# Kernel tuning notes

Measured on AMD Instinct MI355X. Metric: run time of the kernel, lower is better.

## Reference

```python
import jax, jax.numpy as jnp
import numpy as np

C = 512; HEADS = 4; HD = C // HEADS
WS = (5, 9); EXP = (2, 4); FW = (5, 9)
SCALE = HD ** -0.5
B, T, NH, NW = 1, 5, 60, 108

def _valid_ind_rolled():
    wh, ww = WS; eh, ew = EXP
    tl = np.ones((wh, ww)); tl[:-eh, :-ew] = 0
    tr = np.ones((wh, ww)); tr[:-eh, ew:] = 0
    bl = np.ones((wh, ww)); bl[eh:, :-ew] = 0
    br = np.ones((wh, ww)); br[eh:, ew:] = 0
    return np.nonzero(np.stack([tl, tr, bl, br], 0).reshape(-1))[0]

VIR = jnp.asarray(_valid_ind_rolled())  # 120 valid rolled positions

def window_partition(x):
    b, t, h, w, c = x.shape
    x = x.reshape(b, t, h // WS[0], WS[0], w // WS[1], WS[1], c)
    return x.transpose(0, 2, 4, 1, 3, 5, 6).reshape(-1, t * WS[0] * WS[1], c)

def unfold(x, ker, pad):
    # torch.nn.Unfold(kernel=ker, stride=1, padding=pad): (n,c,h,w)->(n,c*kh*kw,L)
    n, c, h, w = x.shape
    xp = jnp.pad(x, ((0, 0), (0, 0), (pad[0], pad[0]), (pad[1], pad[1])))
    oh = h + 2 * pad[0] - ker[0] + 1
    ow = w + 2 * pad[1] - ker[1] + 1
    rows = jnp.arange(oh)[:, None] + jnp.arange(ker[0])[None, :]
    cols = jnp.arange(ow)[:, None] + jnp.arange(ker[1])[None, :]
    p = xp[:, :, rows[:, None, :, None], cols[None, :, None, :]]  # (n,c,oh,ow,kh,kw)
    return p.transpose(0, 1, 4, 5, 2, 3).reshape(n, c * ker[0] * ker[1], oh * ow)

def setup_inputs():
    key = jax.random.key(0)
    ks = jax.random.split(key, 4)
    return {
        "x0": jax.random.normal(ks[0], (B, T, NH, NW, C), jnp.float32),
        "x1": jax.random.normal(ks[1], (B, NH // WS[0], NW // WS[1], T, C), jnp.float32),
        "W_qkv": jax.random.normal(ks[2], (C, 3 * C), jnp.float32) * 0.02,
        "b_qkv": jnp.zeros((3 * C,), jnp.float32),
        "W_proj": jax.random.normal(ks[3], (C, C), jnp.float32) * 0.02,
        "b_proj": jnp.zeros((C,), jnp.float32),
    }

def reference(x0, x1, W_qkv, b_qkv, W_proj, b_proj):
    b, t, nh, nw, c = x0.shape
    wa = t * WS[0] * WS[1]  # tokens per window (225)
    qkv = (x0 @ W_qkv + b_qkv).reshape(b, t, nh, nw, 3, c)
    q, k, v = qkv[..., 0, :], qkv[..., 1, :], qkv[..., 2, :]

    def to_win(z):
        w = window_partition(z).reshape(-1, t, WS[0] * WS[1], HEADS, HD)
        return w.transpose(0, 3, 1, 2, 4).reshape(-1, HEADS, wa, HD)

    q_w, k_w, v_w = to_win(q), to_win(k), to_win(v)

    shifts = [(-EXP[0], -EXP[1]), (-EXP[0], EXP[1]), (EXP[0], -EXP[1]), (EXP[0], EXP[1])]
    def rolled(z):
        parts = [window_partition(jnp.roll(z, s, axis=(2, 3))).reshape(-1, t, WS[0] * WS[1], HEADS, HD) for s in shifts]
        r = jnp.concatenate(parts, axis=2).transpose(0, 3, 1, 2, 4)[:, :, :, VIR]
        return r.reshape(-1, HEADS, t * VIR.shape[0], HD)

    k_rolled = jnp.concatenate([k_w, rolled(k)], 2)
    v_rolled = jnp.concatenate([v_w, rolled(v)], 2)

    # focal level 1 pooling (focal_level=2 -> single unfold level, stride 1)
    xp = x1.transpose(0, 3, 1, 2, 4)  # (B,T,nWh,nWw,C)
    nwh, nww = xp.shape[2], xp.shape[3]
    ker = (2 * (FW[0] // 2) + 1, 2 * (FW[1] // 2) + 1)  # (5,9)
    pad = (ker[0] // 2, ker[1] // 2)
    L = nwh * nww; kk = ker[0] * ker[1]
    um = unfold(jnp.ones((t, 1, nwh, nww), x0.dtype), ker, pad)  # (T,kk,L)
    um = um.reshape(1, t, ker[0], ker[1], L).transpose(4, 1, 2, 3, 0).reshape(L, t * kk)
    pool_mask = jnp.where(um == 0, jnp.float32(-100.0), jnp.float32(0.0))  # (L, T*kk)

    qkv_p = (xp @ W_qkv + b_qkv).reshape(b, t, nwh, nww, 3, c).transpose(4, 0, 1, 5, 2, 3).reshape(3, b * t, c, nwh, nww)
    def pooled(z):
        u = unfold(z, ker, pad).reshape(b, t, c, ker[0], ker[1], L).transpose(0, 5, 1, 3, 4, 2)
        u = u.reshape(-1, t, kk, HEADS, HD).transpose(0, 3, 1, 2, 4)
        return u.reshape(-1, HEADS, t * kk, HD)

    k_all = jnp.concatenate([k_rolled, pooled(qkv_p[1])], 2)
    v_all = jnp.concatenate([v_rolled, pooled(qkv_p[2])], 2)

    attn = jnp.einsum('bhqd,bhkd->bhqk', q_w * SCALE, k_all)
    offset = k_rolled.shape[2]
    pm = jnp.tile(pool_mask[None], (b, 1, 1)).reshape(-1, t * kk)[:, None, None, :]
    attn = attn.at[:, :, :, offset:].add(pm)
    attn = jax.nn.softmax(attn, axis=-1)
    out = jnp.einsum('bhqk,bhkd->bqhd', attn, v_all).reshape(attn.shape[0], wa, c)
    return out @ W_proj + b_proj
```

## Files before the change

kernel.cpp:

```cpp
#include <hip/hip_runtime.h>

typedef _Float16 h16;
typedef __attribute__((ext_vector_type(8))) _Float16 half8;
typedef __attribute__((ext_vector_type(2))) _Float16 half2v;
typedef __attribute__((ext_vector_type(4))) float float4v;

typedef const __attribute__((address_space(1))) unsigned char gu8;
typedef __attribute__((address_space(3))) unsigned char su8;

#define NTOK  32400
#define NPTOK 720
#define CDIM  512
#define SCALE 0.08838834764831845f
#define ZROW  NTOK
#define PROW  (NTOK + 1)

__constant__ int VIR_TBL[120] = {
  5,6,7,8, 14,15,16,17, 23,24,25,26,
  27,28,29,30,31,32,33,34,35, 36,37,38,39,40,41,42,43,44,
  45,46,47,48, 54,55,56,57, 63,64,65,66,
  72,73,74,75,76,77,78,79,80, 81,82,83,84,85,86,87,88,89,
  90,91,92,93,94,95,96,97,98, 99,100,101,102,103,104,105,106,107,
  113,114,115,116, 122,123,124,125, 131,132,133,134,
  135,136,137,138,139,140,141,142,143, 144,145,146,147,148,149,150,151,152,
  153,154,155,156, 162,163,164,165, 171,172,173,174
};

__global__ __launch_bounds__(256) void build_tok(int* __restrict__ Tok,
                                                 int* __restrict__ WMask,
                                                 h16* __restrict__ Kz,
                                                 h16* __restrict__ Vz) {
  const int win = blockIdx.x;
  const int wy = win / 12, wx = win % 12;
  if (win == 0) {
    for (int k = threadIdx.x; k < 512; k += 256) {
      Kz[(size_t)ZROW * CDIM + k] = (h16)0.f;
      Vz[(size_t)ZROW * CDIM + k] = (h16)0.f;
    }
  }
  for (int kidx = threadIdx.x; kidx < 1056; kidx += 256) {
    int e;
    if (kidx < 225) {
      int t = kidx / 45, pos = kidx % 45;
      int y = wy * 5 + pos / 9, x = wx * 9 + pos % 9;
      e = (t * 60 + y) * 108 + x;
    } else if (kidx < 825) {
      int jj = kidx - 225;
      int t = jj / 120, m = jj % 120;
      int vir = VIR_TBL[m];
      int p = vir / 45, pos = vir % 45;
      int r = pos / 9, c = pos % 9;
      int sy = (p < 2) ? -2 : 2;
      int sx = (p & 1) ? 4 : -4;
      int y = (wy * 5 + r - sy + 60) % 60;
      int x = (wx * 9 + c - sx + 108) % 108;
      e = (t * 60 + y) * 108 + x;
    } else if (kidx < 1050) {
      int jp = kidx - 825;
      int t = jp / 45, pos = jp % 45;
      int py = wy + pos / 9 - 2;
      int px = wx + pos % 9 - 4;
      e = (py >= 0 && py < 12 && px >= 0 && px < 12)
            ? (PROW + t * 144 + py * 12 + px) : ZROW;
    } else {
      e = ZROW;
    }
    Tok[win * 1056 + kidx] = e;
  }
  if (threadIdx.x < 33) {
    int m = 0;
#pragma unroll 1
    for (int r = 0; r < 32; r++) {
      int kidx = threadIdx.x * 32 + r;
      bool v;
      if (kidx < 825) v = true;
      else if (kidx < 1050) {
        int jp = kidx - 825, pos = jp % 45;
        int py = wy + pos / 9 - 2, px = wx + pos % 9 - 4;
        v = (py >= 0 && py < 12 && px >= 0 && px < 12);
      } else v = false;
      m |= (v ? 1 : 0) << r;
    }
    WMask[win * 33 + threadIdx.x] = m;
  }
}

__global__ __launch_bounds__(256) void transpose_cvt(const float* __restrict__ src,
                                                     h16* __restrict__ dst,
                                                     int R, int C) {
  __shared__ float T[32][33];
  const int t = threadIdx.x;
  const int ct = blockIdx.x * 32;
  const int rt = blockIdx.y * 32;
  const int c = t & 31, r0 = (t >> 5) * 4;
#pragma unroll
  for (int i = 0; i < 4; i++)
    T[r0 + i][c] = src[(size_t)(rt + r0 + i) * C + ct + c];
  __syncthreads();
#pragma unroll
  for (int i = 0; i < 4; i++)
    dst[(size_t)(ct + r0 + i) * R + rt + c] = (h16)T[c][r0 + i];
}

__global__ __launch_bounds__(256) void cvt_x0(const float* __restrict__ src,
                                              h16* __restrict__ dst) {
  const int total = NTOK * CDIM / 8;
  for (int i = blockIdx.x * 256 + threadIdx.x; i < total; i += gridDim.x * 256) {
    const float4* s = (const float4*)(src + (size_t)i * 8);
    float4 f0 = s[0], f1 = s[1];
    half8 h;
    h[0] = (h16)f0.x; h[1] = (h16)f0.y; h[2] = (h16)f0.z; h[3] = (h16)f0.w;
    h[4] = (h16)f1.x; h[5] = (h16)f1.y; h[6] = (h16)f1.z; h[7] = (h16)f1.w;
    *(half8*)(dst + (size_t)i * 8) = h;
  }
}

struct __align__(16) Stage2 { h16 Ah[2][128][32]; h16 Bh[2][128][32]; };
union __align__(16) GemmLDSQ { Stage2 s; h16 Cs[128][136]; };

__global__ __launch_bounds__(256) void gemm_qkv_mfma(
    const h16* __restrict__ A, const h16* __restrict__ Bt,
    const float* __restrict__ bias,
    h16* __restrict__ Q, h16* __restrict__ K, h16* __restrict__ V)
{
  __shared__ GemmLDSQ u;
  const int tid = threadIdx.x;
  const int lane = tid & 63, wv = tid >> 6;
  const int col = lane & 15, quad = lane >> 4;
  const int bn = blockIdx.x, bm = blockIdx.y;
  const int mo = (wv & 1) * 64, no = (wv >> 1) * 64;

  float4v acc[4][4];
#pragma unroll
  for (int i = 0; i < 4; i++)
#pragma unroll
    for (int j = 0; j < 4; j++) acc[i][j] = (float4v){0.f, 0.f, 0.f, 0.f};

  const int lrow = lane >> 2;
  const int lcol = (((lane & 3) ^ ((lane >> 3) & 3)) * 8);
  const int arow = bm * 128 + wv * 32 + lrow;
  const int ar = arow < NTOK ? arow : (NTOK - 1);
  const int ar2 = (arow + 16) < NTOK ? (arow + 16) : (NTOK - 1);
  const h16* Ag  = A + (size_t)ar * 512 + lcol;
  const h16* Ag2 = A + (size_t)ar2 * 512 + lcol;
  const h16* Bg  = Bt + (size_t)(bn * 128 + wv * 32 + lrow) * 512 + lcol;

#define STAGE_G(buf, k0) do {                                              \
    su8* Al = (su8*)&u.s.Ah[buf][wv * 32][0];                              \
    su8* Bl = (su8*)&u.s.Bh[buf][wv * 32][0];                              \
    __builtin_amdgcn_global_load_lds((gu8*)(Ag + (k0)),            Al,        16, 0, 0); \
    __builtin_amdgcn_global_load_lds((gu8*)(Ag2 + (k0)),           Al + 1024, 16, 0, 0); \
    __builtin_amdgcn_global_load_lds((gu8*)(Bg + (k0)),            Bl,        16, 0, 0); \
    __builtin_amdgcn_global_load_lds((gu8*)(Bg + (k0) + 16 * 512), Bl + 1024, 16, 0, 0); \
  } while (0)

  const int fsw = (quad ^ ((col >> 1) & 3)) * 8;
  STAGE_G(0, 0);
  __syncthreads();
  for (int kt = 0; kt < 16; kt++) {
    const int cur = kt & 1;
    if (kt + 1 < 16) STAGE_G(cur ^ 1, (kt + 1) * 32);

    half8 afr[4], bfr[4];
#pragma unroll
    for (int i = 0; i < 4; i++)
      afr[i] = *(const half8*)&u.s.Ah[cur][mo + i * 16 + col][fsw];
#pragma unroll
    for (int j = 0; j < 4; j++)
      bfr[j] = *(const half8*)&u.s.Bh[cur][no + j * 16 + col][fsw];
#pragma unroll
    for (int i = 0; i < 4; i++)
#pragma unroll
      for (int j = 0; j < 4; j++)
        acc[i][j] = __builtin_amdgcn_mfma_f32_16x16x32_f16(afr[i], bfr[j], acc[i][j], 0, 0, 0);
    __syncthreads();
  }

  float bv[4];
#pragma unroll
  for (int j = 0; j < 4; j++) bv[j] = bias[bn * 128 + no + j * 16 + col];
#pragma unroll
  for (int i = 0; i < 4; i++)
#pragma unroll
    for (int j = 0; j < 4; j++)
#pragma unroll
      for (int r = 0; r < 4; r++)
        u.Cs[mo + i * 16 + quad * 4 + r][no + j * 16 + col] = (h16)(acc[i][j][r] + bv[j]);
  __syncthreads();

  const int row_l = tid >> 1, halfseg = (tid & 1) * 64;
  const int row_g = bm * 128 + row_l;
  const int jsel = bn >> 2;
  const int ch0 = (bn & 3) * 128 + halfseg;
  h16* dst = (jsel == 0) ? Q : (jsel == 1) ? K : V;
  if (row_g < NTOK) {
#pragma unroll
    for (int c = 0; c < 64; c += 8)
      *(half8*)&dst[(size_t)row_g * 512 + ch0 + c] = *(const half8*)&u.Cs[row_l][halfseg + c];
  }
}

__global__ __launch_bounds__(256) void gemm_proj_mfma(
    const h16* __restrict__ A, const h16* __restrict__ Bt,
    const float* __restrict__ bias, float* __restrict__ out)
{
  __shared__ Stage2 s;
  const int tid = threadIdx.x;
  const int lane = tid & 63, wv = tid >> 6;
  const int col = lane & 15, quad = lane >> 4;
  const int bn = blockIdx.x, bm = blockIdx.y;
  const int mo = (wv & 1) * 64, no = (wv >> 1) * 64;

  float4v acc[4][4];
#pragma unroll
  for (int i = 0; i < 4; i++)
#pragma unroll
    for (int j = 0; j < 4; j++) acc[i][j] = (float4v){0.f, 0.f, 0.f, 0.f};

  const int lrow = lane >> 2;
  const int lcol = (((lane & 3) ^ ((lane >> 3) & 3)) * 8);
  const int arow = bm * 128 + wv * 32 + lrow;
  const int ar = arow < NTOK ? arow : (NTOK - 1);
  const int ar2 = (arow + 16) < NTOK ? (arow + 16) : (NTOK - 1);
  const h16* Ag  = A + (size_t)ar * 512 + lcol;
  const h16* Ag2 = A + (size_t)ar2 * 512 + lcol;
  const h16* Bg  = Bt + (size_t)(bn * 128 + wv * 32 + lrow) * 512 + lcol;

#define STAGE_P(buf, k0) do {                                              \
    su8* Al = (su8*)&s.Ah[buf][wv * 32][0];                                \
    su8* Bl = (su8*)&s.Bh[buf][wv * 32][0];                                \
    __builtin_amdgcn_global_load_lds((gu8*)(Ag + (k0)),            Al,        16, 0, 0); \
    __builtin_amdgcn_global_load_lds((gu8*)(Ag2 + (k0)),           Al + 1024, 16, 0, 0); \
    __builtin_amdgcn_global_load_lds((gu8*)(Bg + (k0)),            Bl,        16, 0, 0); \
    __builtin_amdgcn_global_load_lds((gu8*)(Bg + (k0) + 16 * 512), Bl + 1024, 16, 0, 0); \
  } while (0)

  const int fsw = (quad ^ ((col >> 1) & 3)) * 8;
  STAGE_P(0, 0);
  __syncthreads();
  for (int kt = 0; kt < 16; kt++) {
    const int cur = kt & 1;
    if (kt + 1 < 16) STAGE_P(cur ^ 1, (kt + 1) * 32);

    half8 afr[4], bfr[4];
#pragma unroll
    for (int i = 0; i < 4; i++)
      afr[i] = *(const half8*)&s.Ah[cur][mo + i * 16 + col][fsw];
#pragma unroll
    for (int j = 0; j < 4; j++)
      bfr[j] = *(const half8*)&s.Bh[cur][no + j * 16 + col][fsw];
#pragma unroll
    for (int i = 0; i < 4; i++)
#pragma unroll
      for (int j = 0; j < 4; j++)
        acc[i][j] = __builtin_amdgcn_mfma_f32_16x16x32_f16(afr[i], bfr[j], acc[i][j], 0, 0, 0);
    __syncthreads();
  }

  float bv[4];
#pragma unroll
  for (int j = 0; j < 4; j++) bv[j] = bias[bn * 128 + no + j * 16 + col];
#pragma unroll
  for (int i = 0; i < 4; i++) {
#pragma unroll
    for (int r = 0; r < 4; r++) {
      int row_g = bm * 128 + mo + i * 16 + quad * 4 + r;
      if (row_g < NTOK) {
#pragma unroll
        for (int j = 0; j < 4; j++)
          out[(size_t)row_g * 512 + bn * 128 + no + j * 16 + col] = acc[i][j][r] + bv[j];
      }
    }
  }
}

__global__ __launch_bounds__(256) void gemm_pooled(
    const float* __restrict__ A, const float* __restrict__ B,
    const float* __restrict__ bias,
    h16* __restrict__ Kp, h16* __restrict__ Vp)
{
  __shared__ float As[64][17];
  __shared__ float Bs[16][64];
  const int tid = threadIdx.x;
  const int bm = blockIdx.x, bn = blockIdx.y;
  const int tm = tid >> 4, tn = tid & 15;
  const int lrow = tid >> 2, lk = (tid & 3) * 4;
  const int brow = tid >> 4, bcol = (tid & 15) * 4;
  float acc[4][4] = {};
  const int orow = bm * 64 + lrow;
  int srow = 0;
  if (orow < NPTOK) { int t = orow / 144, rem = orow % 144; srow = rem * 5 + t; }
  const float* Ap = A + (size_t)srow * 512 + lk;
  const float* Bp = B + (size_t)brow * 1536 + 512 + bn * 64 + bcol;

  for (int k0 = 0; k0 < 512; k0 += 16) {
    float4 av = make_float4(0.f, 0.f, 0.f, 0.f);
    if (orow < NPTOK) av = *(const float4*)(Ap + k0);
    float4 bv = *(const float4*)(Bp + (size_t)k0 * 1536);
    As[lrow][lk + 0] = av.x; As[lrow][lk + 1] = av.y;
    As[lrow][lk + 2] = av.z; As[lrow][lk + 3] = av.w;
    *(float4*)&Bs[brow][bcol] = bv;
    __syncthreads();
#pragma unroll
    for (int kk = 0; kk < 16; kk++) {
      float a[4];
#pragma unroll
      for (int i = 0; i < 4; i++) a[i] = As[tm * 4 + i][kk];
      float4 b = *(const float4*)&Bs[kk][tn * 4];
#pragma unroll
      for (int i = 0; i < 4; i++) {
        acc[i][0] = fmaf(a[i], b.x, acc[i][0]);
        acc[i][1] = fmaf(a[i], b.y, acc[i][1]);
        acc[i][2] = fmaf(a[i], b.z, acc[i][2]);
        acc[i][3] = fmaf(a[i], b.w, acc[i][3]);
      }
    }
    __syncthreads();
  }
  const int nl = bn * 64 + tn * 4;
  const int j = nl >> 9;
  const int ch = nl & 511;
  h16* dst = (j == 0) ? Kp : Vp;
#pragma unroll
  for (int i = 0; i < 4; i++) {
    int r = bm * 64 + tm * 4 + i;
    if (r < NPTOK) {
#pragma unroll
      for (int c = 0; c < 4; c++)
        dst[(size_t)r * 512 + ch + c] = (h16)(acc[i][c] + bias[512 + nl + c]);
    }
  }
}

__global__ __launch_bounds__(256, 3) void attn_kernel(
    const h16* __restrict__ Qh, const h16* __restrict__ KhU,
    const h16* __restrict__ VhU, const int* __restrict__ Tok,
    const int* __restrict__ WMask, h16* __restrict__ AOh)
{
  __shared__ __align__(16) h16 Ks[2][32 * 136];
  __shared__ __align__(16) h16 Vt[2][128 * 40];

  const int tid = threadIdx.x;
  const int lane = tid & 63;
  const int wv = tid >> 6;
  const int win = blockIdx.x;
  const int head = blockIdx.y;
  const int qg = blockIdx.z;
  const int wy = win / 12, wx = win % 12;
  const int col = lane & 15;
  const int quad = lane >> 4;
  const int* TokW = Tok + win * 1056;
  const int* WMaskW = WMask + win * 33;

  half8 qfrag[2][4];
  const int tile0 = qg * 8 + wv * 2;
#pragma unroll
  for (int tt = 0; tt < 2; tt++) {
    int qrow = (tile0 + tt) * 16 + col;
    if (qrow < 225) {
      int t = qrow / 45, pos = qrow % 45;
      int y = wy * 5 + pos / 9, x = wx * 9 + pos % 9;
      const h16* qsrc = Qh + (size_t)((t * 60 + y) * 108 + x) * CDIM + head * 128;
#pragma unroll
      for (int dc = 0; dc < 4; dc++)
        qfrag[tt][dc] = *(const half8*)(qsrc + dc * 32 + quad * 8);
    } else {
#pragma unroll
      for (int dc = 0; dc < 4; dc++)
#pragma unroll
        for (int jj = 0; jj < 8; jj++) qfrag[tt][dc][jj] = (h16)0.f;
    }
  }

  float4v O[2][8];
#pragma unroll
  for (int tt = 0; tt < 2; tt++)
#pragma unroll
    for (int i = 0; i < 8; i++) O[tt][i] = (float4v){0.f, 0.f, 0.f, 0.f};
  float lp[2] = {0.f, 0.f};

  const int krow = tid >> 3, kseg = tid & 7;
  const int vrp = tid >> 4, vcg = tid & 15;
  const int kch = head * 128 + kseg * 16;
  const int vch = head * 128 + vcg * 8;
  const int rp = (vrp + (vcg & 3) * 4) & 15;

  {
    const h16* ks = KhU + (size_t)TokW[krow] * CDIM + kch;
    half8 k0c = *(const half8*)ks;
    half8 k1c = *(const half8*)(ks + 8);
    half8 vac = *(const half8*)(VhU + (size_t)TokW[2 * vrp] * CDIM + vch);
    half8 vbc = *(const half8*)(VhU + (size_t)TokW[2 * vrp + 1] * CDIM + vch);
    *(half8*)&Ks[0][krow * 136 + kseg * 16] = k0c;
    *(half8*)&Ks[0][krow * 136 + kseg * 16 + 8] = k1c;
#pragma unroll
    for (int i = 0; i < 8; i++) {
      half2v w; w[0] = vac[i]; w[1] = vbc[i];
      *(half2v*)&Vt[0][(vcg * 8 + i) * 40 + rp * 2] = w;
    }
  }
  half8 k0n, k1n, van, vbn;
  {
    const h16* ks = KhU + (size_t)TokW[32 + krow] * CDIM + kch;
    k0n = *(const half8*)ks;
    k1n = *(const half8*)(ks + 8);
    van = *(const half8*)(VhU + (size_t)TokW[32 + 2 * vrp] * CDIM + vch);
    vbn = *(const half8*)(VhU + (size_t)TokW[32 + 2 * vrp + 1] * CDIM + vch);
  }
  int tokK[2], tokVa[2], tokVb[2];
  tokK[0] = TokW[64 + krow]; tokVa[0] = TokW[64 + 2 * vrp]; tokVb[0] = TokW[64 + 2 * vrp + 1];
  tokK[1] = TokW[96 + krow]; tokVa[1] = TokW[96 + 2 * vrp]; tokVb[1] = TokW[96 + 2 * vrp + 1];
  __syncthreads();

  for (int step = 0; step < 33; ++step) {
    const int cur = step & 1;

    if (step + 1 < 33) {
      h16* KsN = Ks[cur ^ 1];
      h16* VtN = Vt[cur ^ 1];
      *(half8*)&KsN[krow * 136 + kseg * 16] = k0n;
      *(half8*)&KsN[krow * 136 + kseg * 16 + 8] = k1n;
#pragma unroll
      for (int i = 0; i < 8; i++) {
        half2v w; w[0] = van[i]; w[1] = vbn[i];
        *(half2v*)&VtN[(vcg * 8 + i) * 40 + rp * 2] = w;
      }
    }
    if (step + 2 < 33) {
      const h16* ks = KhU + (size_t)tokK[cur] * CDIM + kch;
      k0n = *(const half8*)ks;
      k1n = *(const half8*)(ks + 8);
      van = *(const half8*)(VhU + (size_t)tokVa[cur] * CDIM + vch);
      vbn = *(const half8*)(VhU + (size_t)tokVb[cur] * CDIM + vch);
      if (step + 4 < 33) {
        tokK[cur]  = TokW[(step + 4) * 32 + krow];
        tokVa[cur] = TokW[(step + 4) * 32 + 2 * vrp];
        tokVb[cur] = TokW[(step + 4) * 32 + 2 * vrp + 1];
      }
    }

    const int mask = WMaskW[step];
    const h16* KsC = Ks[cur];
    const h16* VtC = Vt[cur];

    float4v s0[2] = {{0.f,0.f,0.f,0.f},{0.f,0.f,0.f,0.f}};
    float4v s1[2] = {{0.f,0.f,0.f,0.f},{0.f,0.f,0.f,0.f}};
    __builtin_amdgcn_s_setprio(1);
#pragma unroll
    for (int dc = 0; dc < 4; dc++) {
      half8 a0 = *(const half8*)&KsC[col * 136 + dc * 32 + quad * 8];
      half8 a1 = *(const half8*)&KsC[(col + 16) * 136 + dc * 32 + quad * 8];
#pragma unroll
      for (int tt = 0; tt < 2; tt++) {
        s0[tt] = __builtin_amdgcn_mfma_f32_16x16x32_f16(a0, qfrag[tt][dc], s0[tt], 0, 0, 0);
        s1[tt] = __builtin_amdgcn_mfma_f32_16x16x32_f16(a1, qfrag[tt][dc], s1[tt], 0, 0, 0);
      }
    }
    __builtin_amdgcn_s_setprio(0);

    half8 pfrag[2];
    const int srcA = (((quad << 1) & 3) << 4) | col;
    const int srcB = ((((quad << 1) + 1) & 3) << 4) | col;
    const bool hi = quad >= 2;
#pragma unroll
    for (int tt = 0; tt < 2; tt++) {
      float pm0[4], pm1[4];
#pragma unroll
      for (int i = 0; i < 4; i++) {
        int r = quad * 4 + i;
        float e0 = __expf(s0[tt][i] * SCALE);
        float e1 = __expf(s1[tt][i] * SCALE);
        pm0[i] = ((mask >> r) & 1) ? e0 : 0.f;
        pm1[i] = ((mask >> (16 + r)) & 1) ? e1 : 0.f;
        lp[tt] += pm0[i] + pm1[i];
      }
      float g00 = __builtin_bit_cast(float, __builtin_amdgcn_cvt_pkrtz(pm0[0], pm0[1]));
      float g01 = __builtin_bit_cast(float, __builtin_amdgcn_cvt_pkrtz(pm0[2], pm0[3]));
      float g10 = __builtin_bit_cast(float, __builtin_amdgcn_cvt_pkrtz(pm1[0], pm1[1]));
      float g11 = __builtin_bit_cast(float, __builtin_amdgcn_cvt_pkrtz(pm1[2], pm1[3]));
      float a0 = __shfl(g00, srcA), a1 = __shfl(g01, srcA);
      float a2 = __shfl(g00, srcB), a3 = __shfl(g01, srcB);
      float b0 = __shfl(g10, srcA), b1 = __shfl(g11, srcA);
      float b2 = __shfl(g10, srcB), b3 = __shfl(g11, srcB);
      float4v pf;
      pf[0] = hi ? b0 : a0;
      pf[1] = hi ? b1 : a1;
      pf[2] = hi ? b2 : a2;
      pf[3] = hi ? b3 : a3;
      pfrag[tt] = __builtin_bit_cast(half8, pf);
    }

    __builtin_amdgcn_s_setprio(1);
#pragma unroll
    for (int dt = 0; dt < 8; dt++) {
      int ch = dt * 16 + col;
      int g4 = ((dt * 2 + (col >> 3)) & 3) * 4;
      int x0 = (quad * 4 + g4) & 15;
      half8 vf = *(const half8*)&VtC[ch * 40 + x0 * 2];
#pragma unroll
      for (int tt = 0; tt < 2; tt++)
        O[tt][dt] = __builtin_amdgcn_mfma_f32_16x16x32_f16(pfrag[tt], vf, O[tt][dt], 0, 0, 0);
    }
    __builtin_amdgcn_s_setprio(0);

    __syncthreads();
  }

#pragma unroll
  for (int tt = 0; tt < 2; tt++) {
    float l_all = lp[tt];
    l_all += __shfl_xor(l_all, 16);
    l_all += __shfl_xor(l_all, 32);
#pragma unroll
    for (int i = 0; i < 4; i++) {
      int qr = (tile0 + tt) * 16 + quad * 4 + i;
      if (qr < 225) {
        float invl = __builtin_amdgcn_rcpf(__shfl(l_all, quad * 4 + i));
        h16* dst = AOh + ((size_t)win * 225 + qr) * CDIM + head * 128 + col;
#pragma unroll
        for (int dt = 0; dt < 8; dt++)
          dst[dt * 16] = (h16)(O[tt][dt][i] * invl);
      }
    }
  }
}

extern "C" void kernel_launch(void* const* d_in, const int* in_sizes, int n_in,
                              void* d_out, int out_size, void* d_ws, size_t ws_size,
                              hipStream_t stream) {
  const float* x0    = (const float*)d_in[0];
  const float* x1    = (const float*)d_in[1];
  const float* Wqkv  = (const float*)d_in[2];
  const float* bqkv  = (const float*)d_in[3];
  const float* Wproj = (const float*)d_in[4];
  const float* bproj = (const float*)d_in[5];
  float* out = (float*)d_out;

  const size_t NU = (size_t)(NTOK + 1 + NPTOK);
  h16* Qh   = (h16*)d_ws;
  h16* KhU  = Qh + (size_t)NTOK * CDIM;
  h16* VhU  = KhU + NU * CDIM;
  h16* Rh   = VhU + NU * CDIM;
  h16* Wqkvt  = Rh + (size_t)NTOK * CDIM;
  h16* Wprojt = Wqkvt + (size_t)1536 * 512;
  int* Tok    = (int*)(Wprojt + (size_t)512 * 512);
  int* WMaskP = Tok + (size_t)144 * 1056;

  build_tok<<<144, 256, 0, stream>>>(Tok, WMaskP, KhU, VhU);
  transpose_cvt<<<dim3(48, 16), 256, 0, stream>>>(Wqkv, Wqkvt, 512, 1536);
  transpose_cvt<<<dim3(16, 16), 256, 0, stream>>>(Wproj, Wprojt, 512, 512);
  cvt_x0<<<2048, 256, 0, stream>>>(x0, Rh);

  gemm_qkv_mfma<<<dim3(12, 254), 256, 0, stream>>>(Rh, Wqkvt, bqkv, Qh, KhU, VhU);
  gemm_pooled<<<dim3(12, 16), 256, 0, stream>>>(x1, Wqkv, bqkv,
                                                KhU + (size_t)PROW * CDIM,
                                                VhU + (size_t)PROW * CDIM);
  attn_kernel<<<dim3(144, 4, 2), 256, 0, stream>>>(Qh, KhU, VhU, Tok, WMaskP, Rh);
  gemm_proj_mfma<<<dim3(4, 254), 256, 0, stream>>>(Rh, Wprojt, bproj, out);
}
```

Measured before the change: 452.1 us.

## Use triple-buffered LDS pipeline with explicit vmcnt waits in both GEMMs

Both the QKV and projection GEMMs switch from a double-buffered LDS staging scheme to three buffers, prefetching two k-tiles ahead. A single explicit vmcnt/lgkmcnt wait plus barrier per step replaces the two __syncthreads per iteration. The aim is to hide global-to-LDS load latency better and cut barrier overhead. In exchange, LDS use per block grows from 32KB to 48KB, which may lower occupancy, and correctness now depends on the hand-written wait counts.

After: 446.6 us. About the same (-1.2%).

```diff
diff --git a/kernel.cpp b/kernel.cpp
--- a/kernel.cpp
+++ b/kernel.cpp
@@ -115,8 +115,8 @@
   }
 }
 
-struct __align__(16) Stage2 { h16 Ah[2][128][32]; h16 Bh[2][128][32]; };
-union __align__(16) GemmLDSQ { Stage2 s; h16 Cs[128][136]; };
+struct __align__(16) Stage3 { h16 Ah[3][128][32]; h16 Bh[3][128][32]; };
+union __align__(16) GemmLDSQ { Stage3 s; h16 Cs[128][136]; };
 
 __global__ __launch_bounds__(256) void gemm_qkv_mfma(
     const h16* __restrict__ A, const h16* __restrict__ Bt,
@@ -154,28 +154,38 @@
     __builtin_amdgcn_global_load_lds((gu8*)(Bg + (k0) + 16 * 512), Bl + 1024, 16, 0, 0); \
   } while (0)
 
+#define QSTEP(bufc, kt, bufs, vmc) do {                                    \
+    asm volatile("s_waitcnt vmcnt(" #vmc ")" ::: "memory");                \
+    asm volatile("s_waitcnt lgkmcnt(0)" ::: "memory");                     \
+    __builtin_amdgcn_s_barrier();                                          \
+    if ((kt) + 2 < 16) STAGE_G(bufs, ((kt) + 2) * 32);                     \
+    half8 afr[4], bfr[4];                                                  \
+    _Pragma("unroll")                                                      \
+    for (int i = 0; i < 4; i++)                                            \
+      afr[i] = *(const half8*)&u.s.Ah[bufc][mo + i * 16 + col][fsw];       \
+    _Pragma("unroll")                                                      \
+    for (int j = 0; j < 4; j++)                                            \
+      bfr[j] = *(const half8*)&u.s.Bh[bufc][no + j * 16 + col][fsw];       \
+    _Pragma("unroll")                                                      \
+    for (int i = 0; i < 4; i++)                                            \
+      _Pragma("unroll")                                                    \
+      for (int j = 0; j < 4; j++)                                          \
+        acc[i][j] = __builtin_amdgcn_mfma_f32_16x16x32_f16(afr[i], bfr[j], acc[i][j], 0, 0, 0); \
+  } while (0)
+
   const int fsw = (quad ^ ((col >> 1) & 3)) * 8;
   STAGE_G(0, 0);
+  STAGE_G(1, 32);
+#pragma unroll 1
+  for (int kb = 0; kb < 5; kb++) {
+    const int kt = kb * 3;
+    QSTEP(0, kt,     2, 4);
+    QSTEP(1, kt + 1, 0, 4);
+    QSTEP(2, kt + 2, 1, 4);
+  }
+  QSTEP(0, 15, 0, 0);
+
   __syncthreads();
-  for (int kt = 0; kt < 16; kt++) {
-    const int cur = kt & 1;
-    if (kt + 1 < 16) STAGE_G(cur ^ 1, (kt + 1) * 32);
-
-    half8 afr[4], bfr[4];
-#pragma unroll
-    for (int i = 0; i < 4; i++)
-      afr[i] = *(const half8*)&u.s.Ah[cur][mo + i * 16 + col][fsw];
-#pragma unroll
-    for (int j = 0; j < 4; j++)
-      bfr[j] = *(const half8*)&u.s.Bh[cur][no + j * 16 + col][fsw];
-#pragma unroll
-    for (int i = 0; i < 4; i++)
-#pragma unroll
-      for (int j = 0; j < 4; j++)
-        acc[i][j] = __builtin_amdgcn_mfma_f32_16x16x32_f16(afr[i], bfr[j], acc[i][j], 0, 0, 0);
-    __syncthreads();
-  }
-
   float bv[4];
 #pragma unroll
   for (int j = 0; j < 4; j++) bv[j] = bias[bn * 128 + no + j * 16 + col];
@@ -204,7 +214,7 @@
     const h16* __restrict__ A, const h16* __restrict__ Bt,
     const float* __restrict__ bias, float* __restrict__ out)
 {
-  __shared__ Stage2 s;
+  __shared__ Stage3 s;
   const int tid = threadIdx.x;
   const int lane = tid & 63, wv = tid >> 6;
   const int col = lane & 15, quad = lane >> 4;
@@ -235,27 +245,36 @@
     __builtin_amdgcn_global_load_lds((gu8*)(Bg + (k0) + 16 * 512), Bl + 1024, 16, 0, 0); \
   } while (0)
 
+#define PSTEP(bufc, kt, bufs, vmc) do {                                    \
+    asm volatile("s_waitcnt vmcnt(" #vmc ")" ::: "memory");                \
+    asm volatile("s_waitcnt lgkmcnt(0)" ::: "memory");                     \
+    __builtin_amdgcn_s_barrier();                                          \
+    if ((kt) + 2 < 16) STAGE_P(bufs, ((kt) + 2) * 32);                     \
+    half8 afr[4], bfr[4];                                                  \
+    _Pragma("unroll")                                                      \
+    for (int i = 0; i < 4; i++)                                            \
+      afr[i] = *(const half8*)&s.Ah[bufc][mo + i * 16 + col][fsw];         \
+    _Pragma("unroll")                                                      \
+    for (int j = 0; j < 4; j++)                                            \
+      bfr[j] = *(const half8*)&s.Bh[bufc][no + j * 16 + col][fsw];         \
+    _Pragma("unroll")                                                      \
+    for (int i = 0; i < 4; i++)                                            \
+      _Pragma("unroll")                                                    \
+      for (int j = 0; j < 4; j++)                                          \
+        acc[i][j] = __builtin_amdgcn_mfma_f32_16x16x32_f16(afr[i], bfr[j], acc[i][j], 0, 0, 0); \
+  } while (0)
+
   const int fsw = (quad ^ ((col >> 1) & 3)) * 8;
   STAGE_P(0, 0);
-  __syncthreads();
-  for (int kt = 0; kt < 16; kt++) {
-    const int cur = kt & 1;
-    if (kt + 1 < 16) STAGE_P(cur ^ 1, (kt + 1) * 32);
-
-    half8 afr[4], bfr[4];
-#pragma unroll
-    for (int i = 0; i < 4; i++)
-      afr[i] = *(const half8*)&s.Ah[cur][mo + i * 16 + col][fsw];
-#pragma unroll
-    for (int j = 0; j < 4; j++)
-      bfr[j] = *(const half8*)&s.Bh[cur][no + j * 16 + col][fsw];
-#pragma unroll
-    for (int i = 0; i < 4; i++)
-#pragma unroll
-      for (int j = 0; j < 4; j++)
-        acc[i][j] = __builtin_amdgcn_mfma_f32_16x16x32_f16(afr[i], bfr[j], acc[i][j], 0, 0, 0);
-    __syncthreads();
-  }
+  STAGE_P(1, 32);
+#pragma unroll 1
+  for (int kb = 0; kb < 5; kb++) {
+    const int kt = kb * 3;
+    PSTEP(0, kt,     2, 4);
+    PSTEP(1, kt + 1, 0, 4);
+    PSTEP(2, kt + 2, 1, 4);
+  }
+  PSTEP(0, 15, 0, 0);
 
   float bv[4];
 #pragma unroll
```
